# Performance work log

Measured on AMD Instinct MI355X. Metric: run time of the kernel, lower is better.

The kernel has to match this reference:

```python
import jax, jax.numpy as jnp
import numpy as np

N_NODES = 100000
N_EDGES = 3200000
EMB_DIM = 128


def setup_inputs() -> dict:
    key = jax.random.key(0)
    k_emb, k_w1, k_w2, k_e = jax.random.split(key, 4)
    emb = jax.random.normal(k_emb, (N_NODES, EMB_DIM), dtype=jnp.float32)
    W1 = jax.random.normal(k_w1, (EMB_DIM, 64), dtype=jnp.float32) * (1.0 / np.sqrt(EMB_DIM))
    b1 = jnp.zeros((64,), dtype=jnp.float32)
    W2 = jax.random.normal(k_w2, (64, 32), dtype=jnp.float32) * (1.0 / np.sqrt(64))
    b2 = jnp.zeros((32,), dtype=jnp.float32)
    edge_index = jax.random.randint(k_e, (2, N_EDGES), 0, N_NODES, dtype=jnp.int64)
    return {"embedding": emb, "W1": W1, "b1": b1, "W2": W2, "b2": b2,
            "edge_index": edge_index}


def gcn_conv(x, W, b, src, dst, n):
    # PyG GCNConv defaults: add self-loops, symmetric normalization D^-1/2 (A+I) D^-1/2,
    # linear transform first, then gather-scale-scatter aggregation, then bias.
    xw = x @ W                                                  # [N, out]
    ones = jnp.ones(src.shape, dtype=xw.dtype)
    deg = jax.ops.segment_sum(ones, dst, num_segments=n) + 1.0  # in-degree + self-loop
    dis = jax.lax.rsqrt(deg)                                    # deg >= 1 always
    norm = dis[src] * dis[dst]                                  # [E]
    agg = jax.ops.segment_sum(xw[src] * norm[:, None], dst, num_segments=n)
    agg = agg + (dis * dis)[:, None] * xw                       # self-loop messages
    return agg + b


def reference(embedding, W1, b1, W2, b2, edge_index):
    n = embedding.shape[0]
    src, dst = edge_index[0], edge_index[1]
    # encode
    h = jax.nn.relu(gcn_conv(embedding, W1, b1, src, dst, n))
    z = gcn_conv(h, W2, b2, src, dst, n)                        # [N, 32]
    # decode: per-edge gather-dot-sigmoid
    logits = jnp.sum(z[src] * z[dst], axis=1)                   # [E]
    return jax.nn.sigmoid(logits)
```

## Files before the change

kernel.cpp:

```cpp
#include <hip/hip_runtime.h>
#include <hip/hip_bf16.h>
#include <math.h>

#define NN 100000
#define NE 3200000
#define NPAD 100096
#define NB 196
#define BN 512
#define EPB 8192
#define NBLK 391

typedef __attribute__((ext_vector_type(8))) short short8;
typedef __attribute__((ext_vector_type(4))) float floatx4;

__device__ __forceinline__ unsigned short bf16_of(float x) {
    __hip_bfloat16 h = __float2bfloat16(x);
    return *(unsigned short*)&h;
}
__device__ __forceinline__ unsigned pack2(float a, float b) {
    return (unsigned)bf16_of(a) | ((unsigned)bf16_of(b) << 16);
}
__device__ __forceinline__ float lo_f(unsigned u) { return __uint_as_float(u << 16); }
__device__ __forceinline__ float hi_f(unsigned u) { return __uint_as_float(u & 0xffff0000u); }
__device__ __forceinline__ void acc8(float* a, uint4 r) {
    a[0] += lo_f(r.x); a[1] += hi_f(r.x);
    a[2] += lo_f(r.y); a[3] += hi_f(r.y);
    a[4] += lo_f(r.z); a[5] += hi_f(r.z);
    a[6] += lo_f(r.w); a[7] += hi_f(r.w);
}

__global__ __launch_bounds__(256) void hist_kernel(const int* __restrict__ dst,
                                                   int* __restrict__ blkhist) {
    __shared__ int cnt[NB];
    int t = threadIdx.x;
    for (int i = t; i < NB; i += 256) cnt[i] = 0;
    __syncthreads();
    int e0 = blockIdx.x * EPB;
    int e1 = min(e0 + EPB, NE);
    for (int e = e0 + t; e < e1; e += 256) atomicAdd(&cnt[dst[e] >> 9], 1);
    __syncthreads();
    for (int i = t; i < NB; i += 256) blkhist[i * NBLK + blockIdx.x] = cnt[i];
}

__global__ __launch_bounds__(64) void scanA_kernel(int* __restrict__ blkhist,
                                                   int* __restrict__ totals) {
    int j = blockIdx.x, lane = threadIdx.x;
    int base = j * NBLK;
    int carry = 0;
    for (int c = 0; c < NBLK; c += 64) {
        int b = c + lane;
        int v = (b < NBLK) ? blkhist[base + b] : 0;
        int inc = v;
#pragma unroll
        for (int m = 1; m < 64; m <<= 1) {
            int u = __shfl_up(inc, m, 64);
            if (lane >= m) inc += u;
        }
        if (b < NBLK) blkhist[base + b] = carry + inc - v;
        carry += __shfl(inc, 63, 64);
    }
    if (lane == 0) totals[j] = carry;
}

__global__ __launch_bounds__(256) void scanB_kernel(const int* __restrict__ totals,
                                                    int* __restrict__ bucket_base) {
    __shared__ int sm[NB];
    int t = threadIdx.x;
    if (t < NB) sm[t] = totals[t];
    __syncthreads();
    if (t == 0) {
        int r = 0;
        for (int i = 0; i < NB; ++i) { bucket_base[i] = r; r += sm[i]; }
        bucket_base[NB] = r;
    }
}

__global__ __launch_bounds__(256) void scatter_kernel(const int* __restrict__ src,
                                                      const int* __restrict__ dst,
                                                      const int* __restrict__ blkhist,
                                                      const int* __restrict__ bucket_base,
                                                      int* __restrict__ staged) {
    __shared__ int cnt[NB];
    __shared__ int lbase[NB + 1];
    __shared__ int gbase[NB];
    __shared__ int sbuf[EPB];
    __shared__ unsigned char sbkt[EPB];
    int t = threadIdx.x;
    for (int i = t; i < NB; i += 256) cnt[i] = 0;
    __syncthreads();
    int e0 = blockIdx.x * EPB;
    int e1 = min(e0 + EPB, NE);
    int cn = e1 - e0;
    for (int e = e0 + t; e < e1; e += 256) atomicAdd(&cnt[dst[e] >> 9], 1);
    __syncthreads();
    if (t < 64) {
        int v[4]; int s = 0;
#pragma unroll
        for (int k = 0; k < 4; ++k) { int idx = t * 4 + k; v[k] = (idx < NB) ? cnt[idx] : 0; s += v[k]; }
        int inc = s;
#pragma unroll
        for (int m = 1; m < 64; m <<= 1) {
            int u = __shfl_up(inc, m, 64);
            if (t >= m) inc += u;
        }
        int run = inc - s;
#pragma unroll
        for (int k = 0; k < 4; ++k) { int idx = t * 4 + k; if (idx < NB) lbase[idx] = run; run += v[k]; }
        if (t == 63) lbase[NB] = inc;
    }
    __syncthreads();
    for (int i = t; i < NB; i += 256) {
        gbase[i] = bucket_base[i] + blkhist[i * NBLK + blockIdx.x];
        cnt[i] = lbase[i];
    }
    __syncthreads();
    for (int e = e0 + t; e < e1; e += 256) {
        int s = src[e], d = dst[e];
        int bk = d >> 9;
        int r = atomicAdd(&cnt[bk], 1);
        sbuf[r] = (s << 9) | (d & (BN - 1));
        sbkt[r] = (unsigned char)bk;
    }
    __syncthreads();
    for (int i = t; i < cn; i += 256) {
        int bk = sbkt[i];
        staged[gbase[bk] + i - lbase[bk]] = sbuf[i];
    }
}

__global__ __launch_bounds__(256) void fine_kernel(const int* __restrict__ staged,
                                                   const int* __restrict__ bucket_base,
                                                   int* __restrict__ offset,
                                                   float* __restrict__ dis,
                                                   int* __restrict__ csr_src) {
    __shared__ int hist[BN];
    __shared__ int offs[BN];
    __shared__ int cur[BN];
    int t = threadIdx.x, j = blockIdx.x;
    int bb = bucket_base[j], be = bucket_base[j + 1];
    for (int i = t; i < BN; i += 256) hist[i] = 0;
    __syncthreads();
    for (int e = bb + t; e < be; e += 256) atomicAdd(&hist[staged[e] & (BN - 1)], 1);
    __syncthreads();
    if (t < 64) {
        int v[8]; int s = 0;
#pragma unroll
        for (int k = 0; k < 8; ++k) { v[k] = hist[t * 8 + k]; s += v[k]; }
        int inc = s;
#pragma unroll
        for (int m = 1; m < 64; m <<= 1) {
            int u = __shfl_up(inc, m, 64);
            if (t >= m) inc += u;
        }
        int run = inc - s;
#pragma unroll
        for (int k = 0; k < 8; ++k) { offs[t * 8 + k] = run; run += v[k]; }
    }
    __syncthreads();
    for (int l = t; l < BN; l += 256) {
        cur[l] = offs[l];
        int n = j * BN + l;
        if (n < NN) {
            offset[n] = bb + offs[l];
            dis[n] = rsqrtf((float)hist[l] + 1.0f);
        }
    }
    if (j == NB - 1 && t == 0) offset[NN] = NE;
    __syncthreads();
    for (int e = bb + t; e < be; e += 256) {
        int p = staged[e];
        int r = atomicAdd(&cur[p & (BN - 1)], 1);
        csr_src[bb + r] = p >> 9;
    }
}

__global__ __launch_bounds__(256) void mm1_kernel(const float* __restrict__ x,
                                                  const float* __restrict__ W,
                                                  const float* __restrict__ dis,
                                                  unsigned short* __restrict__ y) {
    __shared__ unsigned short Wt[64][136];
    int t = threadIdx.x;
    for (int i = t; i < 128 * 64; i += 256) {
        int k = i >> 6, n = i & 63;
        Wt[n][k] = bf16_of(W[i]);
    }
    __syncthreads();
    int wave = t >> 6, lane = t & 63;
    int quad = lane >> 4, n16 = lane & 15;
    short8 bfr[4][4];
#pragma unroll
    for (int s = 0; s < 4; ++s)
#pragma unroll
        for (int tt = 0; tt < 4; ++tt)
            bfr[s][tt] = *(const short8*)&Wt[tt * 16 + n16][s * 32 + quad * 8];
    int tile0 = (blockIdx.x * 4 + wave) * 4;
#pragma unroll 1
    for (int it = 0; it < 4; ++it) {
        int tile = tile0 + it;
        if (tile >= 6250) break;
        int m0 = tile * 16;
        const float* xp = x + (size_t)(m0 + n16) * 128 + quad * 8;
        floatx4 acc0 = {0,0,0,0}, acc1 = {0,0,0,0}, acc2 = {0,0,0,0}, acc3 = {0,0,0,0};
#pragma unroll
        for (int s = 0; s < 4; ++s) {
            float4 lo = *(const float4*)(xp + s * 32);
            float4 hi = *(const float4*)(xp + s * 32 + 4);
            short8 a;
            a[0] = (short)bf16_of(lo.x); a[1] = (short)bf16_of(lo.y);
            a[2] = (short)bf16_of(lo.z); a[3] = (short)bf16_of(lo.w);
            a[4] = (short)bf16_of(hi.x); a[5] = (short)bf16_of(hi.y);
            a[6] = (short)bf16_of(hi.z); a[7] = (short)bf16_of(hi.w);
            acc0 = __builtin_amdgcn_mfma_f32_16x16x32_bf16(a, bfr[s][0], acc0, 0, 0, 0);
            acc1 = __builtin_amdgcn_mfma_f32_16x16x32_bf16(a, bfr[s][1], acc1, 0, 0, 0);
            acc2 = __builtin_amdgcn_mfma_f32_16x16x32_bf16(a, bfr[s][2], acc2, 0, 0, 0);
            acc3 = __builtin_amdgcn_mfma_f32_16x16x32_bf16(a, bfr[s][3], acc3, 0, 0, 0);
        }
#pragma unroll
        for (int r = 0; r < 4; ++r) {
            int ro = m0 + quad * 4 + r;
            float sc = dis[ro];
            unsigned short* yp = y + (size_t)ro * 64 + n16;
            yp[0]  = bf16_of(acc0[r] * sc);
            yp[16] = bf16_of(acc1[r] * sc);
            yp[32] = bf16_of(acc2[r] * sc);
            yp[48] = bf16_of(acc3[r] * sc);
        }
    }
}

__global__ __launch_bounds__(256) void mm2_kernel(const unsigned short* __restrict__ h,
                                                  const float* __restrict__ W,
                                                  const float* __restrict__ dis,
                                                  unsigned short* __restrict__ y) {
    __shared__ unsigned short Wt[32][72];
    int t = threadIdx.x;
    for (int i = t; i < 64 * 32; i += 256) {
        int k = i >> 5, n = i & 31;
        Wt[n][k] = bf16_of(W[i]);
    }
    __syncthreads();
    int wave = t >> 6, lane = t & 63;
    int quad = lane >> 4, n16 = lane & 15;
    short8 bfr[2][2];
#pragma unroll
    for (int s = 0; s < 2; ++s)
#pragma unroll
        for (int tt = 0; tt < 2; ++tt)
            bfr[s][tt] = *(const short8*)&Wt[tt * 16 + n16][s * 32 + quad * 8];
    int tile0 = (blockIdx.x * 4 + wave) * 4;
#pragma unroll 1
    for (int it = 0; it < 4; ++it) {
        int tile = tile0 + it;
        if (tile >= 6250) break;
        int m0 = tile * 16;
        const unsigned short* hp = h + (size_t)(m0 + n16) * 64 + quad * 8;
        floatx4 acc0 = {0,0,0,0}, acc1 = {0,0,0,0};
#pragma unroll
        for (int s = 0; s < 2; ++s) {
            short8 a = *(const short8*)(hp + s * 32);
            acc0 = __builtin_amdgcn_mfma_f32_16x16x32_bf16(a, bfr[s][0], acc0, 0, 0, 0);
            acc1 = __builtin_amdgcn_mfma_f32_16x16x32_bf16(a, bfr[s][1], acc1, 0, 0, 0);
        }
#pragma unroll
        for (int r = 0; r < 4; ++r) {
            int ro = m0 + quad * 4 + r;
            float sc = dis[ro];
            unsigned short* yp = y + (size_t)ro * 32 + n16;
            yp[0]  = bf16_of(acc0[r] * sc);
            yp[16] = bf16_of(acc1[r] * sc);
        }
    }
}

__global__ __launch_bounds__(256) void agg64_kernel(const uint4* __restrict__ ys4,
                                                    const float* __restrict__ dis,
                                                    const int* __restrict__ offset,
                                                    const int* __restrict__ csr_src,
                                                    const float* __restrict__ b,
                                                    uint4* __restrict__ h4) {
    int tid = blockIdx.x * 256 + threadIdx.x;
    int nd = tid >> 3, c = tid & 7;
    if (nd >= NN) return;
    int start = offset[nd], end = offset[nd + 1];
    float acc[8] = {0, 0, 0, 0, 0, 0, 0, 0};
    acc8(acc, ys4[(size_t)nd * 8 + c]);
    int i = start;
    int n8 = start + ((end - start) & ~7);
    for (; i < n8; i += 8) {
        int s0 = csr_src[i],     s1 = csr_src[i + 1], s2 = csr_src[i + 2], s3 = csr_src[i + 3];
        int s4 = csr_src[i + 4], s5 = csr_src[i + 5], s6 = csr_src[i + 6], s7 = csr_src[i + 7];
        uint4 r0 = ys4[(size_t)s0 * 8 + c];
        uint4 r1 = ys4[(size_t)s1 * 8 + c];
        uint4 r2 = ys4[(size_t)s2 * 8 + c];
        uint4 r3 = ys4[(size_t)s3 * 8 + c];
        uint4 r4 = ys4[(size_t)s4 * 8 + c];
        uint4 r5 = ys4[(size_t)s5 * 8 + c];
        uint4 r6 = ys4[(size_t)s6 * 8 + c];
        uint4 r7 = ys4[(size_t)s7 * 8 + c];
        acc8(acc, r0); acc8(acc, r1); acc8(acc, r2); acc8(acc, r3);
        acc8(acc, r4); acc8(acc, r5); acc8(acc, r6); acc8(acc, r7);
    }
    for (; i < end; ++i) acc8(acc, ys4[(size_t)csr_src[i] * 8 + c]);
    float ds = dis[nd];
    const float4 bv0 = *(const float4*)&b[c * 8];
    const float4 bv1 = *(const float4*)&b[c * 8 + 4];
    uint4 o;
    o.x = pack2(fmaxf(fmaf(ds, acc[0], bv0.x), 0.f), fmaxf(fmaf(ds, acc[1], bv0.y), 0.f));
    o.y = pack2(fmaxf(fmaf(ds, acc[2], bv0.z), 0.f), fmaxf(fmaf(ds, acc[3], bv0.w), 0.f));
    o.z = pack2(fmaxf(fmaf(ds, acc[4], bv1.x), 0.f), fmaxf(fmaf(ds, acc[5], bv1.y), 0.f));
    o.w = pack2(fmaxf(fmaf(ds, acc[6], bv1.z), 0.f), fmaxf(fmaf(ds, acc[7], bv1.w), 0.f));
    h4[(size_t)nd * 8 + c] = o;
}

__global__ __launch_bounds__(256) void agg32_kernel(const uint4* __restrict__ ys4,
                                                    const float* __restrict__ dis,
                                                    const int* __restrict__ offset,
                                                    const int* __restrict__ csr_src,
                                                    const float* __restrict__ b,
                                                    uint4* __restrict__ z4) {
    int tid = blockIdx.x * 256 + threadIdx.x;
    int nd = tid >> 2, c = tid & 3;
    if (nd >= NN) return;
    int start = offset[nd], end = offset[nd + 1];
    float acc[8] = {0, 0, 0, 0, 0, 0, 0, 0};
    acc8(acc, ys4[(size_t)nd * 4 + c]);
    int i = start;
    int n8 = start + ((end - start) & ~7);
    for (; i < n8; i += 8) {
        int s0 = csr_src[i],     s1 = csr_src[i + 1], s2 = csr_src[i + 2], s3 = csr_src[i + 3];
        int s4 = csr_src[i + 4], s5 = csr_src[i + 5], s6 = csr_src[i + 6], s7 = csr_src[i + 7];
        uint4 r0 = ys4[(size_t)s0 * 4 + c];
        uint4 r1 = ys4[(size_t)s1 * 4 + c];
        uint4 r2 = ys4[(size_t)s2 * 4 + c];
        uint4 r3 = ys4[(size_t)s3 * 4 + c];
        uint4 r4 = ys4[(size_t)s4 * 4 + c];
        uint4 r5 = ys4[(size_t)s5 * 4 + c];
        uint4 r6 = ys4[(size_t)s6 * 4 + c];
        uint4 r7 = ys4[(size_t)s7 * 4 + c];
        acc8(acc, r0); acc8(acc, r1); acc8(acc, r2); acc8(acc, r3);
        acc8(acc, r4); acc8(acc, r5); acc8(acc, r6); acc8(acc, r7);
    }
    for (; i < end; ++i) acc8(acc, ys4[(size_t)csr_src[i] * 4 + c]);
    float ds = dis[nd];
    const float4 bv0 = *(const float4*)&b[c * 8];
    const float4 bv1 = *(const float4*)&b[c * 8 + 4];
    uint4 o;
    o.x = pack2(fmaf(ds, acc[0], bv0.x), fmaf(ds, acc[1], bv0.y));
    o.y = pack2(fmaf(ds, acc[2], bv0.z), fmaf(ds, acc[3], bv0.w));
    o.z = pack2(fmaf(ds, acc[4], bv1.x), fmaf(ds, acc[5], bv1.y));
    o.w = pack2(fmaf(ds, acc[6], bv1.z), fmaf(ds, acc[7], bv1.w));
    z4[(size_t)nd * 4 + c] = o;
}

__global__ __launch_bounds__(256) void decode_kernel(const uint4* __restrict__ z4,
                                                     const int* __restrict__ src,
                                                     const int* __restrict__ dst,
                                                     float* __restrict__ out) {
    int tid = blockIdx.x * 256 + threadIdx.x;
    int e = tid >> 2, k = tid & 3;
    if (e >= NE) return;
    int s = src[e], d = dst[e];
    uint4 ra = z4[(size_t)s * 4 + k];
    uint4 rb = z4[(size_t)d * 4 + k];
    float acc;
    acc  = lo_f(ra.x) * lo_f(rb.x) + hi_f(ra.x) * hi_f(rb.x);
    acc += lo_f(ra.y) * lo_f(rb.y) + hi_f(ra.y) * hi_f(rb.y);
    acc += lo_f(ra.z) * lo_f(rb.z) + hi_f(ra.z) * hi_f(rb.z);
    acc += lo_f(ra.w) * lo_f(rb.w) + hi_f(ra.w) * hi_f(rb.w);
#pragma unroll
    for (int m = 2; m >= 1; m >>= 1) acc += __shfl_xor(acc, m, 4);
    if (k == 0) out[e] = 1.0f / (1.0f + expf(-acc));
}

extern "C" void kernel_launch(void* const* d_in, const int* in_sizes, int n_in,
                              void* d_out, int out_size, void* d_ws, size_t ws_size,
                              hipStream_t stream) {
    const float* emb = (const float*)d_in[0];
    const float* W1  = (const float*)d_in[1];
    const float* b1  = (const float*)d_in[2];
    const float* W2  = (const float*)d_in[3];
    const float* b2  = (const float*)d_in[4];
    const int*   ei  = (const int*)d_in[5];
    const int* src = ei;
    const int* dst = ei + NE;
    float* out = (float*)d_out;

    char* w = (char*)d_ws;
    int*   offset      = (int*)w;           w += (size_t)NPAD * 4;
    float* dis         = (float*)w;         w += (size_t)NPAD * 4;
    int*   bucket_base = (int*)w;           w += 1024;
    int*   totals      = (int*)w;           w += 1024;
    int*   blkhist     = (int*)w;           w += 307200;
    int*   csr_src     = (int*)w;           w += (size_t)NE * 4;
    int*   staged      = (int*)w;           w += (size_t)NE * 4;
    unsigned short* ysbuf = (unsigned short*)w; w += (size_t)NN * 64 * 2;
    unsigned short* h  = (unsigned short*)w;
    unsigned short* ys1 = ysbuf;
    unsigned short* ys2 = ysbuf;
    unsigned short* z   = ysbuf + (size_t)NN * 32;

    hist_kernel<<<NBLK, 256, 0, stream>>>(dst, blkhist);
    scanA_kernel<<<NB, 64, 0, stream>>>(blkhist, totals);
    scanB_kernel<<<1, 256, 0, stream>>>(totals, bucket_base);
    scatter_kernel<<<NBLK, 256, 0, stream>>>(src, dst, blkhist, bucket_base, staged);
    fine_kernel<<<NB, 256, 0, stream>>>(staged, bucket_base, offset, dis, csr_src);

    mm1_kernel<<<391, 256, 0, stream>>>(emb, W1, dis, ys1);
    agg64_kernel<<<(NN * 8) / 256, 256, 0, stream>>>((const uint4*)ys1, dis, offset, csr_src, b1, (uint4*)h);

    mm2_kernel<<<391, 256, 0, stream>>>(h, W2, dis, ys2);
    agg32_kernel<<<(NN * 4 + 255) / 256, 256, 0, stream>>>((const uint4*)ys2, dis, offset, csr_src, b2, (uint4*)z);

    decode_kernel<<<(NE * 4) / 256, 256, 0, stream>>>((const uint4*)z, src, dst, out);
}
```

Before: 355.8 us.

## Fuse layer-1 aggregation with layer-2 matmul and fold bucket scan into consumers

Layer-1 aggregation now computes the ReLU'd h row in shared memory and immediately multiplies it by W2 in fp32 FMA, writing the dis-scaled layer-2 features. This removes the separate mm2 kernel and the bf16 h round trip through global memory. The single-block scanB kernel is also removed: the scatter and fine kernels each recompute the bucket prefix sum from totals in shared memory. The cost is a scalar 64x32 matmul per node on CUDA cores in place of MFMA, extra shared-memory use, and a redundant scan in every block.

```diff
diff --git a/kernel.cpp b/kernel.cpp
--- a/kernel.cpp
+++ b/kernel.cpp
@@ -12,6 +12,7 @@
 
 typedef __attribute__((ext_vector_type(8))) short short8;
 typedef __attribute__((ext_vector_type(4))) float floatx4;
+typedef __attribute__((ext_vector_type(4))) unsigned uint4v;
 
 __device__ __forceinline__ unsigned short bf16_of(float x) {
     __hip_bfloat16 h = __float2bfloat16(x);
@@ -22,11 +23,11 @@
 }
 __device__ __forceinline__ float lo_f(unsigned u) { return __uint_as_float(u << 16); }
 __device__ __forceinline__ float hi_f(unsigned u) { return __uint_as_float(u & 0xffff0000u); }
-__device__ __forceinline__ void acc8(float* a, uint4 r) {
-    a[0] += lo_f(r.x); a[1] += hi_f(r.x);
-    a[2] += lo_f(r.y); a[3] += hi_f(r.y);
-    a[4] += lo_f(r.z); a[5] += hi_f(r.z);
-    a[6] += lo_f(r.w); a[7] += hi_f(r.w);
+__device__ __forceinline__ void acc8(float* a, uint4v r) {
+    a[0] += lo_f(r[0]); a[1] += hi_f(r[0]);
+    a[2] += lo_f(r[1]); a[3] += hi_f(r[1]);
+    a[4] += lo_f(r[2]); a[5] += hi_f(r[2]);
+    a[6] += lo_f(r[3]); a[7] += hi_f(r[3]);
 }
 
 __global__ __launch_bounds__(256) void hist_kernel(const int* __restrict__ dst,
@@ -62,27 +63,15 @@
     if (lane == 0) totals[j] = carry;
 }
 
-__global__ __launch_bounds__(256) void scanB_kernel(const int* __restrict__ totals,
-                                                    int* __restrict__ bucket_base) {
-    __shared__ int sm[NB];
-    int t = threadIdx.x;
-    if (t < NB) sm[t] = totals[t];
-    __syncthreads();
-    if (t == 0) {
-        int r = 0;
-        for (int i = 0; i < NB; ++i) { bucket_base[i] = r; r += sm[i]; }
-        bucket_base[NB] = r;
-    }
-}
-
 __global__ __launch_bounds__(256) void scatter_kernel(const int* __restrict__ src,
                                                       const int* __restrict__ dst,
                                                       const int* __restrict__ blkhist,
-                                                      const int* __restrict__ bucket_base,
+                                                      const int* __restrict__ totals,
                                                       int* __restrict__ staged) {
     __shared__ int cnt[NB];
     __shared__ int lbase[NB + 1];
     __shared__ int gbase[NB];
+    __shared__ int bbase[NB];
     __shared__ int sbuf[EPB];
     __shared__ unsigned char sbkt[EPB];
     int t = threadIdx.x;
@@ -107,10 +96,22 @@
 #pragma unroll
         for (int k = 0; k < 4; ++k) { int idx = t * 4 + k; if (idx < NB) lbase[idx] = run; run += v[k]; }
         if (t == 63) lbase[NB] = inc;
+        int v2[4]; int s2 = 0;
+#pragma unroll
+        for (int k = 0; k < 4; ++k) { int idx = t * 4 + k; v2[k] = (idx < NB) ? totals[idx] : 0; s2 += v2[k]; }
+        int inc2 = s2;
+#pragma unroll
+        for (int m = 1; m < 64; m <<= 1) {
+            int u = __shfl_up(inc2, m, 64);
+            if (t >= m) inc2 += u;
+        }
+        int run2 = inc2 - s2;
+#pragma unroll
+        for (int k = 0; k < 4; ++k) { int idx = t * 4 + k; if (idx < NB) bbase[idx] = run2; run2 += v2[k]; }
     }
     __syncthreads();
     for (int i = t; i < NB; i += 256) {
-        gbase[i] = bucket_base[i] + blkhist[i * NBLK + blockIdx.x];
+        gbase[i] = bbase[i] + blkhist[i * NBLK + blockIdx.x];
         cnt[i] = lbase[i];
     }
     __syncthreads();
@@ -129,17 +130,33 @@
 }
 
 __global__ __launch_bounds__(256) void fine_kernel(const int* __restrict__ staged,
-                                                   const int* __restrict__ bucket_base,
+                                                   const int* __restrict__ totals,
                                                    int* __restrict__ offset,
                                                    float* __restrict__ dis,
                                                    int* __restrict__ csr_src) {
     __shared__ int hist[BN];
     __shared__ int offs[BN];
     __shared__ int cur[BN];
+    __shared__ int bbase[NB + 1];
     int t = threadIdx.x, j = blockIdx.x;
-    int bb = bucket_base[j], be = bucket_base[j + 1];
+    if (t < 64) {
+        int v2[4]; int s2 = 0;
+#pragma unroll
+        for (int k = 0; k < 4; ++k) { int idx = t * 4 + k; v2[k] = (idx < NB) ? totals[idx] : 0; s2 += v2[k]; }
+        int inc2 = s2;
+#pragma unroll
+        for (int m = 1; m < 64; m <<= 1) {
+            int u = __shfl_up(inc2, m, 64);
+            if (t >= m) inc2 += u;
+        }
+        int run2 = inc2 - s2;
+#pragma unroll
+        for (int k = 0; k < 4; ++k) { int idx = t * 4 + k; if (idx < NB) bbase[idx] = run2; run2 += v2[k]; }
+        if (t == 63) bbase[NB] = inc2;
+    }
     for (int i = t; i < BN; i += 256) hist[i] = 0;
     __syncthreads();
+    int bb = bbase[j], be = bbase[j + 1];
     for (int e = bb + t; e < be; e += 256) atomicAdd(&hist[staged[e] & (BN - 1)], 1);
     __syncthreads();
     if (t < 64) {
@@ -228,59 +245,20 @@
     }
 }
 
-__global__ __launch_bounds__(256) void mm2_kernel(const unsigned short* __restrict__ h,
-                                                  const float* __restrict__ W,
-                                                  const float* __restrict__ dis,
-                                                  unsigned short* __restrict__ y) {
-    __shared__ unsigned short Wt[32][72];
+__global__ __launch_bounds__(256) void agg64mm2_kernel(const uint4v* __restrict__ ys4,
+                                                       const float* __restrict__ dis,
+                                                       const int* __restrict__ offset,
+                                                       const int* __restrict__ csr_src,
+                                                       const float* __restrict__ b1,
+                                                       const float* __restrict__ W2,
+                                                       unsigned int* __restrict__ ys2) {
+    __shared__ float w2s[64 * 32];
+    __shared__ float hbuf[32 * 68];
     int t = threadIdx.x;
-    for (int i = t; i < 64 * 32; i += 256) {
-        int k = i >> 5, n = i & 31;
-        Wt[n][k] = bf16_of(W[i]);
-    }
-    __syncthreads();
-    int wave = t >> 6, lane = t & 63;
-    int quad = lane >> 4, n16 = lane & 15;
-    short8 bfr[2][2];
-#pragma unroll
-    for (int s = 0; s < 2; ++s)
-#pragma unroll
-        for (int tt = 0; tt < 2; ++tt)
-            bfr[s][tt] = *(const short8*)&Wt[tt * 16 + n16][s * 32 + quad * 8];
-    int tile0 = (blockIdx.x * 4 + wave) * 4;
-#pragma unroll 1
-    for (int it = 0; it < 4; ++it) {
-        int tile = tile0 + it;
-        if (tile >= 6250) break;
-        int m0 = tile * 16;
-        const unsigned short* hp = h + (size_t)(m0 + n16) * 64 + quad * 8;
-        floatx4 acc0 = {0,0,0,0}, acc1 = {0,0,0,0};
-#pragma unroll
-        for (int s = 0; s < 2; ++s) {
-            short8 a = *(const short8*)(hp + s * 32);
-            acc0 = __builtin_amdgcn_mfma_f32_16x16x32_bf16(a, bfr[s][0], acc0, 0, 0, 0);
-            acc1 = __builtin_amdgcn_mfma_f32_16x16x32_bf16(a, bfr[s][1], acc1, 0, 0, 0);
-        }
-#pragma unroll
-        for (int r = 0; r < 4; ++r) {
-            int ro = m0 + quad * 4 + r;
-            float sc = dis[ro];
-            unsigned short* yp = y + (size_t)ro * 32 + n16;
-            yp[0]  = bf16_of(acc0[r] * sc);
-            yp[16] = bf16_of(acc1[r] * sc);
-        }
-    }
-}
-
-__global__ __launch_bounds__(256) void agg64_kernel(const uint4* __restrict__ ys4,
-                                                    const float* __restrict__ dis,
-                                                    const int* __restrict__ offset,
-                                                    const int* __restrict__ csr_src,
-                                                    const float* __restrict__ b,
-                                                    uint4* __restrict__ h4) {
-    int tid = blockIdx.x * 256 + threadIdx.x;
+    for (int i = t; i < 2048; i += 256) w2s[i] = W2[i];
+    __syncthreads();
+    int tid = blockIdx.x * 256 + t;
     int nd = tid >> 3, c = tid & 7;
-    if (nd >= NN) return;
     int start = offset[nd], end = offset[nd + 1];
     float acc[8] = {0, 0, 0, 0, 0, 0, 0, 0};
     acc8(acc, ys4[(size_t)nd * 8 + c]);
@@ -289,35 +267,55 @@
     for (; i < n8; i += 8) {
         int s0 = csr_src[i],     s1 = csr_src[i + 1], s2 = csr_src[i + 2], s3 = csr_src[i + 3];
         int s4 = csr_src[i + 4], s5 = csr_src[i + 5], s6 = csr_src[i + 6], s7 = csr_src[i + 7];
-        uint4 r0 = ys4[(size_t)s0 * 8 + c];
-        uint4 r1 = ys4[(size_t)s1 * 8 + c];
-        uint4 r2 = ys4[(size_t)s2 * 8 + c];
-        uint4 r3 = ys4[(size_t)s3 * 8 + c];
-        uint4 r4 = ys4[(size_t)s4 * 8 + c];
-        uint4 r5 = ys4[(size_t)s5 * 8 + c];
-        uint4 r6 = ys4[(size_t)s6 * 8 + c];
-        uint4 r7 = ys4[(size_t)s7 * 8 + c];
+        uint4v r0 = ys4[(size_t)s0 * 8 + c];
+        uint4v r1 = ys4[(size_t)s1 * 8 + c];
+        uint4v r2 = ys4[(size_t)s2 * 8 + c];
+        uint4v r3 = ys4[(size_t)s3 * 8 + c];
+        uint4v r4 = ys4[(size_t)s4 * 8 + c];
+        uint4v r5 = ys4[(size_t)s5 * 8 + c];
+        uint4v r6 = ys4[(size_t)s6 * 8 + c];
+        uint4v r7 = ys4[(size_t)s7 * 8 + c];
         acc8(acc, r0); acc8(acc, r1); acc8(acc, r2); acc8(acc, r3);
         acc8(acc, r4); acc8(acc, r5); acc8(acc, r6); acc8(acc, r7);
     }
     for (; i < end; ++i) acc8(acc, ys4[(size_t)csr_src[i] * 8 + c]);
     float ds = dis[nd];
-    const float4 bv0 = *(const float4*)&b[c * 8];
-    const float4 bv1 = *(const float4*)&b[c * 8 + 4];
-    uint4 o;
-    o.x = pack2(fmaxf(fmaf(ds, acc[0], bv0.x), 0.f), fmaxf(fmaf(ds, acc[1], bv0.y), 0.f));
-    o.y = pack2(fmaxf(fmaf(ds, acc[2], bv0.z), 0.f), fmaxf(fmaf(ds, acc[3], bv0.w), 0.f));
-    o.z = pack2(fmaxf(fmaf(ds, acc[4], bv1.x), 0.f), fmaxf(fmaf(ds, acc[5], bv1.y), 0.f));
-    o.w = pack2(fmaxf(fmaf(ds, acc[6], bv1.z), 0.f), fmaxf(fmaf(ds, acc[7], bv1.w), 0.f));
-    h4[(size_t)nd * 8 + c] = o;
-}
-
-__global__ __launch_bounds__(256) void agg32_kernel(const uint4* __restrict__ ys4,
+    const float4 bv0 = *(const float4*)&b1[c * 8];
+    const float4 bv1 = *(const float4*)&b1[c * 8 + 4];
+    float* hrow = &hbuf[(t >> 3) * 68];
+    float4 h0, h1;
+    h0.x = fmaxf(fmaf(ds, acc[0], bv0.x), 0.f);
+    h0.y = fmaxf(fmaf(ds, acc[1], bv0.y), 0.f);
+    h0.z = fmaxf(fmaf(ds, acc[2], bv0.z), 0.f);
+    h0.w = fmaxf(fmaf(ds, acc[3], bv0.w), 0.f);
+    h1.x = fmaxf(fmaf(ds, acc[4], bv1.x), 0.f);
+    h1.y = fmaxf(fmaf(ds, acc[5], bv1.y), 0.f);
+    h1.z = fmaxf(fmaf(ds, acc[6], bv1.z), 0.f);
+    h1.w = fmaxf(fmaf(ds, acc[7], bv1.w), 0.f);
+    *(float4*)&hrow[c * 8]     = h0;
+    *(float4*)&hrow[c * 8 + 4] = h1;
+    float p0 = 0.f, p1 = 0.f, p2 = 0.f, p3 = 0.f;
+#pragma unroll 8
+    for (int k = 0; k < 64; ++k) {
+        float hk = hrow[k];
+        const float4 wr = *(const float4*)&w2s[k * 32 + c * 4];
+        p0 = fmaf(hk, wr.x, p0);
+        p1 = fmaf(hk, wr.y, p1);
+        p2 = fmaf(hk, wr.z, p2);
+        p3 = fmaf(hk, wr.w, p3);
+    }
+    p0 *= ds; p1 *= ds; p2 *= ds; p3 *= ds;
+    unsigned int* zp = ys2 + (size_t)nd * 16 + c * 2;
+    zp[0] = pack2(p0, p1);
+    zp[1] = pack2(p2, p3);
+}
+
+__global__ __launch_bounds__(256) void agg32_kernel(const uint4v* __restrict__ ys4,
                                                     const float* __restrict__ dis,
                                                     const int* __restrict__ offset,
                                                     const int* __restrict__ csr_src,
                                                     const float* __restrict__ b,
-                                                    uint4* __restrict__ z4) {
+                                                    uint4v* __restrict__ z4) {
     int tid = blockIdx.x * 256 + threadIdx.x;
     int nd = tid >> 2, c = tid & 3;
     if (nd >= NN) return;
@@ -329,14 +327,14 @@
     for (; i < n8; i += 8) {
         int s0 = csr_src[i],     s1 = csr_src[i + 1], s2 = csr_src[i + 2], s3 = csr_src[i + 3];
         int s4 = csr_src[i + 4], s5 = csr_src[i + 5], s6 = csr_src[i + 6], s7 = csr_src[i + 7];
-        uint4 r0 = ys4[(size_t)s0 * 4 + c];
-        uint4 r1 = ys4[(size_t)s1 * 4 + c];
-        uint4 r2 = ys4[(size_t)s2 * 4 + c];
-        uint4 r3 = ys4[(size_t)s3 * 4 + c];
-        uint4 r4 = ys4[(size_t)s4 * 4 + c];
-        uint4 r5 = ys4[(size_t)s5 * 4 + c];
-        uint4 r6 = ys4[(size_t)s6 * 4 + c];
-        uint4 r7 = ys4[(size_t)s7 * 4 + c];
+        uint4v r0 = ys4[(size_t)s0 * 4 + c];
+        uint4v r1 = ys4[(size_t)s1 * 4 + c];
+        uint4v r2 = ys4[(size_t)s2 * 4 + c];
+        uint4v r3 = ys4[(size_t)s3 * 4 + c];
+        uint4v r4 = ys4[(size_t)s4 * 4 + c];
+        uint4v r5 = ys4[(size_t)s5 * 4 + c];
+        uint4v r6 = ys4[(size_t)s6 * 4 + c];
+        uint4v r7 = ys4[(size_t)s7 * 4 + c];
         acc8(acc, r0); acc8(acc, r1); acc8(acc, r2); acc8(acc, r3);
         acc8(acc, r4); acc8(acc, r5); acc8(acc, r6); acc8(acc, r7);
     }
@@ -344,15 +342,15 @@
     float ds = dis[nd];
     const float4 bv0 = *(const float4*)&b[c * 8];
     const float4 bv1 = *(const float4*)&b[c * 8 + 4];
-    uint4 o;
-    o.x = pack2(fmaf(ds, acc[0], bv0.x), fmaf(ds, acc[1], bv0.y));
-    o.y = pack2(fmaf(ds, acc[2], bv0.z), fmaf(ds, acc[3], bv0.w));
-    o.z = pack2(fmaf(ds, acc[4], bv1.x), fmaf(ds, acc[5], bv1.y));
-    o.w = pack2(fmaf(ds, acc[6], bv1.z), fmaf(ds, acc[7], bv1.w));
+    uint4v o;
+    o[0] = pack2(fmaf(ds, acc[0], bv0.x), fmaf(ds, acc[1], bv0.y));
+    o[1] = pack2(fmaf(ds, acc[2], bv0.z), fmaf(ds, acc[3], bv0.w));
+    o[2] = pack2(fmaf(ds, acc[4], bv1.x), fmaf(ds, acc[5], bv1.y));
+    o[3] = pack2(fmaf(ds, acc[6], bv1.z), fmaf(ds, acc[7], bv1.w));
     z4[(size_t)nd * 4 + c] = o;
 }
 
-__global__ __launch_bounds__(256) void decode_kernel(const uint4* __restrict__ z4,
+__global__ __launch_bounds__(256) void decode_kernel(const uint4v* __restrict__ z4,
                                                      const int* __restrict__ src,
                                                      const int* __restrict__ dst,
                                                      float* __restrict__ out) {
@@ -360,13 +358,13 @@
     int e = tid >> 2, k = tid & 3;
     if (e >= NE) return;
     int s = src[e], d = dst[e];
-    uint4 ra = z4[(size_t)s * 4 + k];
-    uint4 rb = z4[(size_t)d * 4 + k];
+    uint4v ra = z4[(size_t)s * 4 + k];
+    uint4v rb = z4[(size_t)d * 4 + k];
     float acc;
-    acc  = lo_f(ra.x) * lo_f(rb.x) + hi_f(ra.x) * hi_f(rb.x);
-    acc += lo_f(ra.y) * lo_f(rb.y) + hi_f(ra.y) * hi_f(rb.y);
-    acc += lo_f(ra.z) * lo_f(rb.z) + hi_f(ra.z) * hi_f(rb.z);
-    acc += lo_f(ra.w) * lo_f(rb.w) + hi_f(ra.w) * hi_f(rb.w);
+    acc  = lo_f(ra[0]) * lo_f(rb[0]) + hi_f(ra[0]) * hi_f(rb[0]);
+    acc += lo_f(ra[1]) * lo_f(rb[1]) + hi_f(ra[1]) * hi_f(rb[1]);
+    acc += lo_f(ra[2]) * lo_f(rb[2]) + hi_f(ra[2]) * hi_f(rb[2]);
+    acc += lo_f(ra[3]) * lo_f(rb[3]) + hi_f(ra[3]) * hi_f(rb[3]);
 #pragma unroll
     for (int m = 2; m >= 1; m >>= 1) acc += __shfl_xor(acc, m, 4);
     if (k == 0) out[e] = 1.0f / (1.0f + expf(-acc));
@@ -388,28 +386,24 @@
     char* w = (char*)d_ws;
     int*   offset      = (int*)w;           w += (size_t)NPAD * 4;
     float* dis         = (float*)w;         w += (size_t)NPAD * 4;
-    int*   bucket_base = (int*)w;           w += 1024;
     int*   totals      = (int*)w;           w += 1024;
     int*   blkhist     = (int*)w;           w += 307200;
     int*   csr_src     = (int*)w;           w += (size_t)NE * 4;
     int*   staged      = (int*)w;           w += (size_t)NE * 4;
     unsigned short* ysbuf = (unsigned short*)w; w += (size_t)NN * 64 * 2;
-    unsigned short* h  = (unsigned short*)w;
+    unsigned short* ys2 = (unsigned short*)w;
     unsigned short* ys1 = ysbuf;
-    unsigned short* ys2 = ysbuf;
-    unsigned short* z   = ysbuf + (size_t)NN * 32;
+    unsigned short* z   = ysbuf;
 
     hist_kernel<<<NBLK, 256, 0, stream>>>(dst, blkhist);
     scanA_kernel<<<NB, 64, 0, stream>>>(blkhist, totals);
-    scanB_kernel<<<1, 256, 0, stream>>>(totals, bucket_base);
-    scatter_kernel<<<NBLK, 256, 0, stream>>>(src, dst, blkhist, bucket_base, staged);
-    fine_kernel<<<NB, 256, 0, stream>>>(staged, bucket_base, offset, dis, csr_src);
+    scatter_kernel<<<NBLK, 256, 0, stream>>>(src, dst, blkhist, totals, staged);
+    fine_kernel<<<NB, 256, 0, stream>>>(staged, totals, offset, dis, csr_src);
 
     mm1_kernel<<<391, 256, 0, stream>>>(emb, W1, dis, ys1);
-    agg64_kernel<<<(NN * 8) / 256, 256, 0, stream>>>((const uint4*)ys1, dis, offset, csr_src, b1, (uint4*)h);
-
-    mm2_kernel<<<391, 256, 0, stream>>>(h, W2, dis, ys2);
-    agg32_kernel<<<(NN * 4 + 255) / 256, 256, 0, stream>>>((const uint4*)ys2, dis, offset, csr_src, b2, (uint4*)z);
-
-    decode_kernel<<<(NE * 4) / 256, 256, 0, stream>>>((const uint4*)z, src, dst, out);
-}
+    agg64mm2_kernel<<<(NN * 8) / 256, 256, 0, stream>>>((const uint4v*)ys1, dis, offset, csr_src,
+                                                        b1, W2, (unsigned int*)ys2);
+    agg32_kernel<<<(NN * 4 + 255) / 256, 256, 0, stream>>>((const uint4v*)ys2, dis, offset, csr_src, b2, (uint4v*)z);
+
+    decode_kernel<<<(NE * 4) / 256, 256, 0, stream>>>((const uint4v*)z, src, dst, out);
+}
```

Result: no change. 351.9 us (-1.1%).
